# Optimization experiments

Hardware: AMD Instinct MI355X
Metric: run time of the kernel (lower is better)

The kernel has to match this reference:

```python
import jax, jax.numpy as jnp
import numpy as np

B, C, H, W = 64, 64, 128, 128


def setup_inputs() -> dict:
    key = jax.random.key(0)
    x = jax.random.normal(key, (B, C, H, W), dtype=jnp.float32)
    return {"x": x, "topk": 256}


def reference(x, topk):
    b = x.shape[0]
    xf = x.reshape(b, -1)                      # [B, N]
    _, idx = jax.lax.top_k(jnp.abs(xf), topk)  # [B, K] indices of largest |x|
    vals = jnp.take_along_axis(xf, idx, axis=-1)  # gather original (signed) values
    rows = jnp.arange(b)[:, None]
    out = jnp.zeros_like(xf).at[rows, idx].set(vals)  # scatter into zeros
    return out.reshape(x.shape)
```

## Files before the change

### kernel.cpp

```cpp
#include <hip/hip_runtime.h>
#include <stdint.h>


#define NBINS   4096
#define TBINS   2048
#define TB_BASE 2048u
#define G_COLLECT 2052u
#define ROWS  64
#define HBLK  8
#define CBLK  4
#define LC_CAP 4096
#define LDS_SEL 2048

__global__ __launch_bounds__(512) void hist_collect_kernel(
    const float* __restrict__ x, unsigned* __restrict__ parts,
    unsigned* __restrict__ cand_count, uint2* __restrict__ cand, unsigned cap1,
    unsigned* __restrict__ row_over, int n_per_row)
{
    __shared__ unsigned lh[TBINS];
    __shared__ uint2 lc[LC_CAP];
    __shared__ unsigned lcnt;
    __shared__ unsigned gbase;
    for (int i = threadIdx.x; i < TBINS; i += blockDim.x) lh[i] = 0;
    if (threadIdx.x == 0) lcnt = 0;
    __syncthreads();

    int row = blockIdx.x / HBLK;
    int sub = blockIdx.x % HBLK;
    int chunk = n_per_row / HBLK;
    const float4* xv = (const float4*)(x + (size_t)row * n_per_row + (size_t)sub * chunk);
    unsigned idx_base = (unsigned)(sub * chunk);
    int nvec = chunk / 4;
    for (int i = threadIdx.x; i < nvec; i += blockDim.x) {
        float4 v = xv[i];
        unsigned bb[4] = {__float_as_uint(v.x), __float_as_uint(v.y),
                          __float_as_uint(v.z), __float_as_uint(v.w)};
        #pragma unroll
        for (int c = 0; c < 4; ++c) {
            unsigned bin = (bb[c] & 0x7fffffffu) >> 19;
            if (bin >= TB_BASE) {
                atomicAdd(&lh[bin - TB_BASE], 1u);
                if (bin >= G_COLLECT) {
                    unsigned pos = atomicAdd(&lcnt, 1u);
                    if (pos < (unsigned)LC_CAP)
                        lc[pos] = make_uint2(bb[c],
                                             idx_base + (unsigned)i * 4u + (unsigned)c);
                }
            }
        }
    }
    __syncthreads();

    unsigned* gp = parts + (size_t)blockIdx.x * TBINS;
    for (int i = threadIdx.x; i < TBINS; i += blockDim.x) gp[i] = lh[i];

    unsigned n = lcnt;
    if (threadIdx.x == 0) {
        unsigned nn = (n > (unsigned)LC_CAP) ? (unsigned)LC_CAP : n;
        gbase = atomicAdd(&cand_count[row], nn);
        if (n > (unsigned)LC_CAP || gbase + nn > cap1) atomicOr(&row_over[row], 1u);
    }
    if (n > (unsigned)LC_CAP) n = (unsigned)LC_CAP;
    __syncthreads();
    unsigned base = gbase;
    for (unsigned i = threadIdx.x; i < n; i += blockDim.x) {
        unsigned p = base + i;
        if (p < cap1) cand[(size_t)row * cap1 + p] = lc[i];
    }
}

__global__ __launch_bounds__(256) void cutoff_kernel(
    const unsigned* __restrict__ parts, const int* __restrict__ topk,
    const unsigned* __restrict__ row_over,
    unsigned* __restrict__ row_b, unsigned* __restrict__ row_r,
    unsigned* __restrict__ row_ok)
{
    __shared__ unsigned h[TBINS];
    __shared__ unsigned csum[256];
    int row = blockIdx.x;
    const unsigned* base = parts + (size_t)row * HBLK * TBINS;
    for (int i = threadIdx.x; i < TBINS; i += blockDim.x) {
        unsigned s = 0;
        #pragma unroll
        for (int p = 0; p < HBLK; ++p) s += base[(size_t)p * TBINS + i];
        h[i] = s;
    }
    __syncthreads();

    const int CHUNK = TBINS / 256;
    unsigned cs = 0;
    int cbase = threadIdx.x * CHUNK;
    #pragma unroll
    for (int j = 0; j < CHUNK; ++j) cs += h[cbase + j];
    csum[threadIdx.x] = cs;
    __syncthreads();

    if (threadIdx.x == 0) {
        unsigned K = (unsigned)(*topk);
        unsigned acc = 0;
        int found = 0, ch;
        for (ch = 255; ch >= 0; --ch) {
            if (acc + csum[ch] >= K) { found = 1; break; }
            acc += csum[ch];
        }
        unsigned okf = 0;
        if (found) {
            int b = ch * CHUNK + CHUNK - 1;
            for (; b > ch * CHUNK; --b) {
                unsigned c = h[b];
                if (acc + c >= K) break;
                acc += c;
            }
            unsigned bstar = (unsigned)b + TB_BASE;
            row_b[row] = bstar;
            row_r[row] = K - acc;
            okf = (bstar >= G_COLLECT && row_over[row] == 0) ? 1u : 0u;
        }
        row_ok[row] = okf;
    }
}

__global__ __launch_bounds__(256) void compact_kernel(
    const unsigned* __restrict__ cand_count, const uint2* __restrict__ cand,
    unsigned cap1, const unsigned* __restrict__ row_ok,
    const unsigned* __restrict__ row_b,
    unsigned* __restrict__ cand2_count, uint2* __restrict__ cand2, unsigned cap2,
    float* __restrict__ out, int n_per_row)
{
    int row = blockIdx.x / CBLK;
    if (!row_ok[row]) return;
    unsigned bstar = row_b[row];
    unsigned M = cand_count[row]; if (M > cap1) M = cap1;
    const uint2* c = cand + (size_t)row * cap1;
    int sub = blockIdx.x % CBLK;
    for (unsigned i = (unsigned)sub * blockDim.x + threadIdx.x; i < M;
         i += blockDim.x * CBLK) {
        uint2 e = c[i];
        unsigned bin = (e.x & 0x7fffffffu) >> 19;
        if (bin > bstar) {
            out[(size_t)row * n_per_row + e.y] = __uint_as_float(e.x);
        } else if (bin == bstar) {
            unsigned pos = atomicAdd(&cand2_count[row], 1u);
            if (pos < cap2) cand2[(size_t)row * cap2 + pos] = e;
        }
    }
}

__global__ __launch_bounds__(256) void fallback_kernel(
    const float* __restrict__ x, const int* __restrict__ topk,
    const unsigned* __restrict__ row_ok, unsigned* __restrict__ row_r,
    unsigned* __restrict__ cand2_count, uint2* __restrict__ cand2, unsigned cap2,
    float* __restrict__ out, int n_per_row)
{
    __shared__ unsigned h[NBINS];
    __shared__ unsigned csum[256];
    __shared__ unsigned sb;
    int row = blockIdx.x;
    if (row_ok[row]) return;

    for (int i = threadIdx.x; i < NBINS; i += blockDim.x) h[i] = 0;
    __syncthreads();
    const float* xr = x + (size_t)row * n_per_row;
    for (int i = threadIdx.x; i < n_per_row; i += blockDim.x)
        atomicAdd(&h[(__float_as_uint(xr[i]) & 0x7fffffffu) >> 19], 1u);
    __syncthreads();

    const int CHUNK = NBINS / 256;
    unsigned cs = 0;
    for (int j = 0; j < CHUNK; ++j) cs += h[threadIdx.x * CHUNK + j];
    csum[threadIdx.x] = cs;
    __syncthreads();

    if (threadIdx.x == 0) {
        unsigned K = (unsigned)(*topk);
        unsigned acc = 0;
        int ch = 255;
        for (; ch > 0; --ch) { if (acc + csum[ch] >= K) break; acc += csum[ch]; }
        int b = ch * CHUNK + CHUNK - 1;
        for (; b > ch * CHUNK; --b) {
            unsigned c = h[b];
            if (acc + c >= K) break;
            acc += c;
        }
        sb = (unsigned)b;
        row_r[row] = K - acc;
    }
    __syncthreads();

    unsigned bstar = sb;
    for (int i = threadIdx.x; i < n_per_row; i += blockDim.x) {
        unsigned bits = __float_as_uint(xr[i]);
        unsigned bin = (bits & 0x7fffffffu) >> 19;
        if (bin > bstar) {
            out[(size_t)row * n_per_row + i] = __uint_as_float(bits);
        } else if (bin == bstar) {
            unsigned pos = atomicAdd(&cand2_count[row], 1u);
            if (pos < cap2) cand2[(size_t)row * cap2 + pos] = make_uint2(bits, (unsigned)i);
        }
    }
}

__global__ __launch_bounds__(256) void select_kernel(
    const unsigned* __restrict__ cand2_count, const uint2* __restrict__ cand2,
    unsigned cap2, const unsigned* __restrict__ row_r,
    float* __restrict__ out, int n_per_row)
{
    __shared__ uint2 lc[LDS_SEL];
    int row = blockIdx.x;
    unsigned M = cand2_count[row];
    if (M > cap2) M = cap2;
    unsigned r = row_r[row];
    const uint2* c = cand2 + (size_t)row * cap2;
    if (M <= LDS_SEL) {
        for (unsigned i = threadIdx.x; i < M; i += blockDim.x) lc[i] = c[i];
        __syncthreads();
        for (unsigned i = threadIdx.x; i < M; i += blockDim.x) {
            uint2 ci = lc[i];
            unsigned ai = ci.x & 0x7fffffffu;
            unsigned rank = 0;
            for (unsigned j = 0; j < M; ++j) {
                uint2 cj = lc[j];
                unsigned aj = cj.x & 0x7fffffffu;
                rank += (unsigned)((aj > ai) || (aj == ai && cj.y < ci.y));
            }
            if (rank < r)
                out[(size_t)row * n_per_row + ci.y] = __uint_as_float(ci.x);
        }
    } else {
        for (unsigned i = threadIdx.x; i < M; i += blockDim.x) {
            uint2 ci = c[i];
            unsigned ai = ci.x & 0x7fffffffu;
            unsigned rank = 0;
            for (unsigned j = 0; j < M; ++j) {
                uint2 cj = c[j];
                unsigned aj = cj.x & 0x7fffffffu;
                rank += (unsigned)((aj > ai) || (aj == ai && cj.y < ci.y));
            }
            if (rank < r)
                out[(size_t)row * n_per_row + ci.y] = __uint_as_float(ci.x);
        }
    }
}

extern "C" void kernel_launch(void* const* d_in, const int* in_sizes, int n_in,
                              void* d_out, int out_size, void* d_ws, size_t ws_size,
                              hipStream_t stream) {
    const float* x  = (const float*)d_in[0];
    const int* topk = (const int*)d_in[1];
    float* out      = (float*)d_out;

    const int rows = ROWS;
    const int n_per_row = out_size / rows;

    uint8_t* ws = (uint8_t*)d_ws;
    size_t off = 0;
    unsigned* parts = (unsigned*)(ws + off);
    off += (size_t)rows * HBLK * TBINS * sizeof(unsigned);
    unsigned* cand_count  = (unsigned*)(ws + off); off += 256;
    unsigned* cand2_count = (unsigned*)(ws + off); off += 256;
    unsigned* row_over    = (unsigned*)(ws + off); off += 256;
    unsigned* row_b       = (unsigned*)(ws + off); off += 256;
    unsigned* row_r       = (unsigned*)(ws + off); off += 256;
    unsigned* row_ok      = (unsigned*)(ws + off); off += 256;
    off = (off + 255) & ~(size_t)255;

    size_t avail = (ws_size > off) ? (ws_size - off) : 0;
    size_t entries = avail / ((size_t)rows * sizeof(uint2));
    unsigned cap1 = 32768u, cap2 = 16384u;
    if (entries < (size_t)(cap1 + cap2)) {
        cap2 = (unsigned)(entries / 3); if (cap2 == 0) cap2 = 1;
        cap1 = (unsigned)(entries - cap2); if (cap1 == 0) cap1 = 1;
    }
    uint2* cand  = (uint2*)(ws + off); off += (size_t)rows * cap1 * sizeof(uint2);
    uint2* cand2 = (uint2*)(ws + off);

    hipMemsetAsync((void*)cand_count, 0, 768, stream);
    hipMemsetAsync((void*)out, 0, (size_t)out_size * sizeof(float), stream);

    hist_collect_kernel<<<rows * HBLK, 512, 0, stream>>>(x, parts, cand_count, cand,
                                                         cap1, row_over, n_per_row);
    cutoff_kernel<<<rows, 256, 0, stream>>>(parts, topk, row_over, row_b, row_r, row_ok);
    compact_kernel<<<rows * CBLK, 256, 0, stream>>>(cand_count, cand, cap1, row_ok,
                                                    row_b, cand2_count, cand2, cap2,
                                                    out, n_per_row);
    fallback_kernel<<<rows, 256, 0, stream>>>(x, topk, row_ok, row_r,
                                              cand2_count, cand2, cap2, out, n_per_row);
    select_kernel<<<rows, 256, 0, stream>>>(cand2_count, cand2, cap2, row_r,
                                            out, n_per_row);
}
```

Measured before the change: 513.0 us.

## Fuse output zeroing into histogram pass and merge compact with select

The output zero-fill moves into the histogram/collect kernel, which streams x anyway and now writes zeros to out, so the separate memset is gone. Candidate lists become per-block slices with no global atomics, and the histogram shrinks to 512 clamped top bins. The compact and select kernels merge into one per-row kernel that buffers boundary-bin candidates in LDS and ranks them there. The fallback gains multi-level radix refinement, and one launch plus a memset are removed at the cost of fewer blocks for compaction.

```diff
diff --git a/kernel.cpp b/kernel.cpp
--- a/kernel.cpp
+++ b/kernel.cpp
@@ -2,25 +2,45 @@
 #include <stdint.h>
 
 
-#define NBINS   4096
-#define TBINS   2048
+#define TBINS   512
 #define TB_BASE 2048u
+#define TOPBIN  (TB_BASE + TBINS - 1)
 #define G_COLLECT 2052u
 #define ROWS  64
 #define HBLK  8
-#define CBLK  4
-#define LC_CAP 4096
+#define NBLKS (ROWS * HBLK)
+#define CAP_DEF 4096u
 #define LDS_SEL 2048
+#define OVERFLAG 0x80000000u
+
+__device__ inline unsigned clamped_bin(unsigned bits) {
+    unsigned b = (bits & 0x7fffffffu) >> 19;
+    return b > TOPBIN ? TOPBIN : b;
+}
+
+__device__ inline void rank_select(const uint2* sel, unsigned M, unsigned r,
+                                   float* orow) {
+    for (unsigned i = threadIdx.x; i < M; i += blockDim.x) {
+        uint2 ci = sel[i];
+        unsigned ai = ci.x & 0x7fffffffu;
+        unsigned rank = 0;
+        for (unsigned j = 0; j < M; ++j) {
+            uint2 cj = sel[j];
+            unsigned aj = cj.x & 0x7fffffffu;
+            rank += (unsigned)((aj > ai) || (aj == ai && cj.y < ci.y));
+        }
+        if (rank < r) orow[ci.y] = __uint_as_float(ci.x);
+    }
+}
 
 __global__ __launch_bounds__(512) void hist_collect_kernel(
-    const float* __restrict__ x, unsigned* __restrict__ parts,
-    unsigned* __restrict__ cand_count, uint2* __restrict__ cand, unsigned cap1,
-    unsigned* __restrict__ row_over, int n_per_row)
+    const float* __restrict__ x, float* __restrict__ out,
+    unsigned* __restrict__ parts, unsigned* __restrict__ bcount,
+    uint2* __restrict__ cand, unsigned cap, int n_per_row)
 {
     __shared__ unsigned lh[TBINS];
-    __shared__ uint2 lc[LC_CAP];
+    __shared__ uint2 lc[CAP_DEF];
     __shared__ unsigned lcnt;
-    __shared__ unsigned gbase;
     for (int i = threadIdx.x; i < TBINS; i += blockDim.x) lh[i] = 0;
     if (threadIdx.x == 0) lcnt = 0;
     __syncthreads();
@@ -28,21 +48,25 @@
     int row = blockIdx.x / HBLK;
     int sub = blockIdx.x % HBLK;
     int chunk = n_per_row / HBLK;
-    const float4* xv = (const float4*)(x + (size_t)row * n_per_row + (size_t)sub * chunk);
+    size_t base_e = (size_t)row * n_per_row + (size_t)sub * chunk;
+    const float4* xv = (const float4*)(x + base_e);
+    float4* ov = (float4*)(out + base_e);
     unsigned idx_base = (unsigned)(sub * chunk);
+    const float4 z = make_float4(0.f, 0.f, 0.f, 0.f);
     int nvec = chunk / 4;
     for (int i = threadIdx.x; i < nvec; i += blockDim.x) {
         float4 v = xv[i];
+        ov[i] = z;
         unsigned bb[4] = {__float_as_uint(v.x), __float_as_uint(v.y),
                           __float_as_uint(v.z), __float_as_uint(v.w)};
         #pragma unroll
         for (int c = 0; c < 4; ++c) {
-            unsigned bin = (bb[c] & 0x7fffffffu) >> 19;
-            if (bin >= TB_BASE) {
-                atomicAdd(&lh[bin - TB_BASE], 1u);
-                if (bin >= G_COLLECT) {
+            unsigned cb = clamped_bin(bb[c]);
+            if (cb >= TB_BASE) {
+                atomicAdd(&lh[cb - TB_BASE], 1u);
+                if (cb >= G_COLLECT) {
                     unsigned pos = atomicAdd(&lcnt, 1u);
-                    if (pos < (unsigned)LC_CAP)
+                    if (pos < CAP_DEF)
                         lc[pos] = make_uint2(bb[c],
                                              idx_base + (unsigned)i * 4u + (unsigned)c);
                 }
@@ -55,28 +79,21 @@
     for (int i = threadIdx.x; i < TBINS; i += blockDim.x) gp[i] = lh[i];
 
     unsigned n = lcnt;
-    if (threadIdx.x == 0) {
-        unsigned nn = (n > (unsigned)LC_CAP) ? (unsigned)LC_CAP : n;
-        gbase = atomicAdd(&cand_count[row], nn);
-        if (n > (unsigned)LC_CAP || gbase + nn > cap1) atomicOr(&row_over[row], 1u);
-    }
-    if (n > (unsigned)LC_CAP) n = (unsigned)LC_CAP;
-    __syncthreads();
-    unsigned base = gbase;
-    for (unsigned i = threadIdx.x; i < n; i += blockDim.x) {
-        unsigned p = base + i;
-        if (p < cap1) cand[(size_t)row * cap1 + p] = lc[i];
-    }
+    unsigned lim = (cap < CAP_DEF) ? cap : CAP_DEF;
+    unsigned nn = (n > lim) ? lim : n;
+    if (threadIdx.x == 0)
+        bcount[blockIdx.x] = nn | ((n > lim) ? OVERFLAG : 0u);
+    uint2* cp = cand + (size_t)blockIdx.x * cap;
+    for (unsigned i = threadIdx.x; i < nn; i += blockDim.x) cp[i] = lc[i];
 }
 
 __global__ __launch_bounds__(256) void cutoff_kernel(
-    const unsigned* __restrict__ parts, const int* __restrict__ topk,
-    const unsigned* __restrict__ row_over,
+    const unsigned* __restrict__ parts, const unsigned* __restrict__ bcount,
+    const int* __restrict__ topk,
     unsigned* __restrict__ row_b, unsigned* __restrict__ row_r,
     unsigned* __restrict__ row_ok)
 {
     __shared__ unsigned h[TBINS];
-    __shared__ unsigned csum[256];
     int row = blockIdx.x;
     const unsigned* base = parts + (size_t)row * HBLK * TBINS;
     for (int i = threadIdx.x; i < TBINS; i += blockDim.x) {
@@ -87,158 +104,188 @@
     }
     __syncthreads();
 
-    const int CHUNK = TBINS / 256;
-    unsigned cs = 0;
-    int cbase = threadIdx.x * CHUNK;
-    #pragma unroll
-    for (int j = 0; j < CHUNK; ++j) cs += h[cbase + j];
-    csum[threadIdx.x] = cs;
-    __syncthreads();
-
     if (threadIdx.x == 0) {
+        unsigned over = 0;
+        #pragma unroll
+        for (int p = 0; p < HBLK; ++p) over |= bcount[row * HBLK + p] & OVERFLAG;
         unsigned K = (unsigned)(*topk);
         unsigned acc = 0;
-        int found = 0, ch;
-        for (ch = 255; ch >= 0; --ch) {
-            if (acc + csum[ch] >= K) { found = 1; break; }
-            acc += csum[ch];
+        int b = TBINS - 1, found = 0;
+        for (; b >= 0; --b) {
+            if (acc + h[b] >= K) { found = 1; break; }
+            acc += h[b];
         }
         unsigned okf = 0;
         if (found) {
-            int b = ch * CHUNK + CHUNK - 1;
-            for (; b > ch * CHUNK; --b) {
-                unsigned c = h[b];
-                if (acc + c >= K) break;
-                acc += c;
-            }
             unsigned bstar = (unsigned)b + TB_BASE;
             row_b[row] = bstar;
             row_r[row] = K - acc;
-            okf = (bstar >= G_COLLECT && row_over[row] == 0) ? 1u : 0u;
+            okf = (bstar >= G_COLLECT && !over) ? 1u : 0u;
         }
         row_ok[row] = okf;
     }
 }
 
-__global__ __launch_bounds__(256) void compact_kernel(
-    const unsigned* __restrict__ cand_count, const uint2* __restrict__ cand,
-    unsigned cap1, const unsigned* __restrict__ row_ok,
-    const unsigned* __restrict__ row_b,
-    unsigned* __restrict__ cand2_count, uint2* __restrict__ cand2, unsigned cap2,
-    float* __restrict__ out, int n_per_row)
+__global__ __launch_bounds__(256) void compact_select_kernel(
+    const unsigned* __restrict__ bcount, const uint2* __restrict__ cand,
+    unsigned cap, const unsigned* __restrict__ row_ok,
+    const unsigned* __restrict__ row_b, const unsigned* __restrict__ row_r,
+    unsigned* __restrict__ row_fb, float* __restrict__ out, int n_per_row)
 {
-    int row = blockIdx.x / CBLK;
-    if (!row_ok[row]) return;
-    unsigned bstar = row_b[row];
-    unsigned M = cand_count[row]; if (M > cap1) M = cap1;
-    const uint2* c = cand + (size_t)row * cap1;
-    int sub = blockIdx.x % CBLK;
-    for (unsigned i = (unsigned)sub * blockDim.x + threadIdx.x; i < M;
-         i += blockDim.x * CBLK) {
-        uint2 e = c[i];
-        unsigned bin = (e.x & 0x7fffffffu) >> 19;
-        if (bin > bstar) {
-            out[(size_t)row * n_per_row + e.y] = __uint_as_float(e.x);
-        } else if (bin == bstar) {
-            unsigned pos = atomicAdd(&cand2_count[row], 1u);
-            if (pos < cap2) cand2[(size_t)row * cap2 + pos] = e;
-        }
-    }
+    __shared__ uint2 sel[LDS_SEL];
+    __shared__ unsigned scnt;
+    int row = blockIdx.x;
+    unsigned fb = 1;
+    if (row_ok[row]) {
+        unsigned bstar = row_b[row];
+        unsigned r = row_r[row];
+        float* orow = out + (size_t)row * n_per_row;
+        if (threadIdx.x == 0) scnt = 0;
+        __syncthreads();
+        for (int p = 0; p < HBLK; ++p) {
+            unsigned n = bcount[row * HBLK + p] & ~OVERFLAG;
+            const uint2* cp = cand + (size_t)(row * HBLK + p) * cap;
+            for (unsigned i = threadIdx.x; i < n; i += blockDim.x) {
+                uint2 e = cp[i];
+                unsigned bin = clamped_bin(e.x);
+                if (bin > bstar) {
+                    orow[e.y] = __uint_as_float(e.x);
+                } else if (bin == bstar) {
+                    unsigned pos = atomicAdd(&scnt, 1u);
+                    if (pos < LDS_SEL) sel[pos] = e;
+                }
+            }
+        }
+        __syncthreads();
+        unsigned M = scnt;
+        if (M <= LDS_SEL) {
+            rank_select(sel, M, r, orow);
+            fb = 0;
+        }
+    }
+    if (threadIdx.x == 0) row_fb[row] = fb;
 }
 
 __global__ __launch_bounds__(256) void fallback_kernel(
     const float* __restrict__ x, const int* __restrict__ topk,
-    const unsigned* __restrict__ row_ok, unsigned* __restrict__ row_r,
-    unsigned* __restrict__ cand2_count, uint2* __restrict__ cand2, unsigned cap2,
-    float* __restrict__ out, int n_per_row)
+    const unsigned* __restrict__ row_fb, float* __restrict__ out, int n_per_row)
 {
-    __shared__ unsigned h[NBINS];
-    __shared__ unsigned csum[256];
-    __shared__ unsigned sb;
     int row = blockIdx.x;
-    if (row_ok[row]) return;
-
-    for (int i = threadIdx.x; i < NBINS; i += blockDim.x) h[i] = 0;
-    __syncthreads();
+    if (!row_fb[row]) return;
+
+    __shared__ unsigned h[4096];
+    __shared__ uint2 sel[LDS_SEL];
+    __shared__ unsigned sb, sr, scnt, runbase;
+    __shared__ unsigned sc[256];
     const float* xr = x + (size_t)row * n_per_row;
+    float* orow = out + (size_t)row * n_per_row;
+    unsigned K = (unsigned)(*topk);
+
+    for (int i = threadIdx.x; i < 4096; i += blockDim.x) h[i] = 0;
+    __syncthreads();
     for (int i = threadIdx.x; i < n_per_row; i += blockDim.x)
         atomicAdd(&h[(__float_as_uint(xr[i]) & 0x7fffffffu) >> 19], 1u);
     __syncthreads();
-
-    const int CHUNK = NBINS / 256;
-    unsigned cs = 0;
-    for (int j = 0; j < CHUNK; ++j) cs += h[threadIdx.x * CHUNK + j];
-    csum[threadIdx.x] = cs;
-    __syncthreads();
-
     if (threadIdx.x == 0) {
-        unsigned K = (unsigned)(*topk);
-        unsigned acc = 0;
-        int ch = 255;
-        for (; ch > 0; --ch) { if (acc + csum[ch] >= K) break; acc += csum[ch]; }
-        int b = ch * CHUNK + CHUNK - 1;
-        for (; b > ch * CHUNK; --b) {
-            unsigned c = h[b];
-            if (acc + c >= K) break;
-            acc += c;
-        }
-        sb = (unsigned)b;
-        row_r[row] = K - acc;
-    }
-    __syncthreads();
-
-    unsigned bstar = sb;
+        unsigned acc = 0; int b = 4095;
+        for (; b > 0; --b) { if (acc + h[b] >= K) break; acc += h[b]; }
+        sb = (unsigned)b; sr = K - acc; scnt = 0;
+    }
+    __syncthreads();
+    unsigned bstar = sb, r = sr;
     for (int i = threadIdx.x; i < n_per_row; i += blockDim.x) {
         unsigned bits = __float_as_uint(xr[i]);
         unsigned bin = (bits & 0x7fffffffu) >> 19;
-        if (bin > bstar) {
-            out[(size_t)row * n_per_row + i] = __uint_as_float(bits);
-        } else if (bin == bstar) {
-            unsigned pos = atomicAdd(&cand2_count[row], 1u);
-            if (pos < cap2) cand2[(size_t)row * cap2 + pos] = make_uint2(bits, (unsigned)i);
-        }
-    }
-}
-
-__global__ __launch_bounds__(256) void select_kernel(
-    const unsigned* __restrict__ cand2_count, const uint2* __restrict__ cand2,
-    unsigned cap2, const unsigned* __restrict__ row_r,
-    float* __restrict__ out, int n_per_row)
-{
-    __shared__ uint2 lc[LDS_SEL];
-    int row = blockIdx.x;
-    unsigned M = cand2_count[row];
-    if (M > cap2) M = cap2;
-    unsigned r = row_r[row];
-    const uint2* c = cand2 + (size_t)row * cap2;
-    if (M <= LDS_SEL) {
-        for (unsigned i = threadIdx.x; i < M; i += blockDim.x) lc[i] = c[i];
-        __syncthreads();
-        for (unsigned i = threadIdx.x; i < M; i += blockDim.x) {
-            uint2 ci = lc[i];
-            unsigned ai = ci.x & 0x7fffffffu;
-            unsigned rank = 0;
-            for (unsigned j = 0; j < M; ++j) {
-                uint2 cj = lc[j];
-                unsigned aj = cj.x & 0x7fffffffu;
-                rank += (unsigned)((aj > ai) || (aj == ai && cj.y < ci.y));
-            }
-            if (rank < r)
-                out[(size_t)row * n_per_row + ci.y] = __uint_as_float(ci.x);
-        }
-    } else {
-        for (unsigned i = threadIdx.x; i < M; i += blockDim.x) {
-            uint2 ci = c[i];
-            unsigned ai = ci.x & 0x7fffffffu;
-            unsigned rank = 0;
-            for (unsigned j = 0; j < M; ++j) {
-                uint2 cj = c[j];
-                unsigned aj = cj.x & 0x7fffffffu;
-                rank += (unsigned)((aj > ai) || (aj == ai && cj.y < ci.y));
-            }
-            if (rank < r)
-                out[(size_t)row * n_per_row + ci.y] = __uint_as_float(ci.x);
-        }
+        if (bin > bstar) orow[i] = __uint_as_float(bits);
+        else if (bin == bstar) {
+            unsigned p = atomicAdd(&scnt, 1u);
+            if (p < LDS_SEL) sel[p] = make_uint2(bits, (unsigned)i);
+        }
+    }
+    __syncthreads();
+    if (scnt <= LDS_SEL) { rank_select(sel, scnt, r, orow); return; }
+
+    for (int i = threadIdx.x; i < 2048; i += blockDim.x) h[i] = 0;
+    __syncthreads();
+    for (int i = threadIdx.x; i < n_per_row; i += blockDim.x) {
+        unsigned bits = __float_as_uint(xr[i]);
+        if (((bits & 0x7fffffffu) >> 19) == bstar)
+            atomicAdd(&h[(bits >> 8) & 0x7ffu], 1u);
+    }
+    __syncthreads();
+    if (threadIdx.x == 0) {
+        unsigned acc = 0; int s = 2047;
+        for (; s > 0; --s) { if (acc + h[s] >= r) break; acc += h[s]; }
+        sb = (unsigned)s; sr = r - acc; scnt = 0;
+    }
+    __syncthreads();
+    unsigned s1 = sb; r = sr;
+    for (int i = threadIdx.x; i < n_per_row; i += blockDim.x) {
+        unsigned bits = __float_as_uint(xr[i]);
+        if (((bits & 0x7fffffffu) >> 19) != bstar) continue;
+        unsigned sub = (bits >> 8) & 0x7ffu;
+        if (sub > s1) orow[i] = __uint_as_float(bits);
+        else if (sub == s1) {
+            unsigned p = atomicAdd(&scnt, 1u);
+            if (p < LDS_SEL) sel[p] = make_uint2(bits, (unsigned)i);
+        }
+    }
+    __syncthreads();
+    if (scnt <= LDS_SEL) { rank_select(sel, scnt, r, orow); return; }
+
+    for (int i = threadIdx.x; i < 256; i += blockDim.x) h[i] = 0;
+    __syncthreads();
+    for (int i = threadIdx.x; i < n_per_row; i += blockDim.x) {
+        unsigned bits = __float_as_uint(xr[i]);
+        if (((bits & 0x7fffffffu) >> 19) == bstar && ((bits >> 8) & 0x7ffu) == s1)
+            atomicAdd(&h[bits & 0xffu], 1u);
+    }
+    __syncthreads();
+    if (threadIdx.x == 0) {
+        unsigned acc = 0; int s = 255;
+        for (; s > 0; --s) { if (acc + h[s] >= r) break; acc += h[s]; }
+        sb = (unsigned)s; sr = r - acc; scnt = 0;
+    }
+    __syncthreads();
+    unsigned s2 = sb; r = sr;
+    for (int i = threadIdx.x; i < n_per_row; i += blockDim.x) {
+        unsigned bits = __float_as_uint(xr[i]);
+        if (((bits & 0x7fffffffu) >> 19) != bstar || ((bits >> 8) & 0x7ffu) != s1)
+            continue;
+        unsigned sub = bits & 0xffu;
+        if (sub > s2) orow[i] = __uint_as_float(bits);
+        else if (sub == s2) {
+            unsigned p = atomicAdd(&scnt, 1u);
+            if (p < LDS_SEL) sel[p] = make_uint2(bits, (unsigned)i);
+        }
+    }
+    __syncthreads();
+    if (scnt <= LDS_SEL) { rank_select(sel, scnt, r, orow); return; }
+
+    unsigned tabs = ((bstar << 19) | (s1 << 8) | s2) & 0x7fffffffu;
+    if (threadIdx.x == 0) runbase = 0;
+    __syncthreads();
+    for (int base = 0; base < n_per_row; base += 256) {
+        if (runbase >= r) break;
+        int i = base + (int)threadIdx.x;
+        unsigned bits = 0, m = 0;
+        if (i < n_per_row) {
+            bits = __float_as_uint(xr[i]);
+            m = ((bits & 0x7fffffffu) == tabs) ? 1u : 0u;
+        }
+        sc[threadIdx.x] = m;
+        __syncthreads();
+        for (int st = 1; st < 256; st <<= 1) {
+            unsigned v = (threadIdx.x >= (unsigned)st) ? sc[threadIdx.x - st] : 0u;
+            __syncthreads();
+            sc[threadIdx.x] += v;
+            __syncthreads();
+        }
+        unsigned excl = sc[threadIdx.x] - m;
+        if (m && (runbase + excl) < r) orow[i] = __uint_as_float(bits);
+        __syncthreads();
+        if (threadIdx.x == 0) runbase += sc[255];
+        __syncthreads();
     }
 }
 
@@ -254,37 +301,25 @@
 
     uint8_t* ws = (uint8_t*)d_ws;
     size_t off = 0;
-    unsigned* parts = (unsigned*)(ws + off);
-    off += (size_t)rows * HBLK * TBINS * sizeof(unsigned);
-    unsigned* cand_count  = (unsigned*)(ws + off); off += 256;
-    unsigned* cand2_count = (unsigned*)(ws + off); off += 256;
-    unsigned* row_over    = (unsigned*)(ws + off); off += 256;
-    unsigned* row_b       = (unsigned*)(ws + off); off += 256;
-    unsigned* row_r       = (unsigned*)(ws + off); off += 256;
-    unsigned* row_ok      = (unsigned*)(ws + off); off += 256;
+    unsigned* parts  = (unsigned*)(ws + off);
+    off += (size_t)NBLKS * TBINS * sizeof(unsigned);
+    unsigned* bcount = (unsigned*)(ws + off); off += (NBLKS * 4 + 255) & ~255u;
+    unsigned* row_b  = (unsigned*)(ws + off); off += 256;
+    unsigned* row_r  = (unsigned*)(ws + off); off += 256;
+    unsigned* row_ok = (unsigned*)(ws + off); off += 256;
+    unsigned* row_fb = (unsigned*)(ws + off); off += 256;
     off = (off + 255) & ~(size_t)255;
 
     size_t avail = (ws_size > off) ? (ws_size - off) : 0;
-    size_t entries = avail / ((size_t)rows * sizeof(uint2));
-    unsigned cap1 = 32768u, cap2 = 16384u;
-    if (entries < (size_t)(cap1 + cap2)) {
-        cap2 = (unsigned)(entries / 3); if (cap2 == 0) cap2 = 1;
-        cap1 = (unsigned)(entries - cap2); if (cap1 == 0) cap1 = 1;
-    }
-    uint2* cand  = (uint2*)(ws + off); off += (size_t)rows * cap1 * sizeof(uint2);
-    uint2* cand2 = (uint2*)(ws + off);
-
-    hipMemsetAsync((void*)cand_count, 0, 768, stream);
-    hipMemsetAsync((void*)out, 0, (size_t)out_size * sizeof(float), stream);
-
-    hist_collect_kernel<<<rows * HBLK, 512, 0, stream>>>(x, parts, cand_count, cand,
-                                                         cap1, row_over, n_per_row);
-    cutoff_kernel<<<rows, 256, 0, stream>>>(parts, topk, row_over, row_b, row_r, row_ok);
-    compact_kernel<<<rows * CBLK, 256, 0, stream>>>(cand_count, cand, cap1, row_ok,
-                                                    row_b, cand2_count, cand2, cap2,
-                                                    out, n_per_row);
-    fallback_kernel<<<rows, 256, 0, stream>>>(x, topk, row_ok, row_r,
-                                              cand2_count, cand2, cap2, out, n_per_row);
-    select_kernel<<<rows, 256, 0, stream>>>(cand2_count, cand2, cap2, row_r,
-                                            out, n_per_row);
-}
+    size_t per_blk = avail / ((size_t)NBLKS * sizeof(uint2));
+    unsigned cap = (per_blk > CAP_DEF) ? CAP_DEF : (unsigned)per_blk;
+    if (cap == 0) cap = 1;
+    uint2* cand = (uint2*)(ws + off);
+
+    hist_collect_kernel<<<NBLKS, 512, 0, stream>>>(x, out, parts, bcount, cand,
+                                                   cap, n_per_row);
+    cutoff_kernel<<<rows, 256, 0, stream>>>(parts, bcount, topk, row_b, row_r, row_ok);
+    compact_select_kernel<<<rows, 256, 0, stream>>>(bcount, cand, cap, row_ok,
+                                                    row_b, row_r, row_fb, out, n_per_row);
+    fallback_kernel<<<rows, 256, 0, stream>>>(x, topk, row_fb, out, n_per_row);
+}
```

Result: no change. 507.2 us (-1.1%).
